# Kernel tuning notes

Hardware: AMD Instinct MI355X
Metric: run time of the kernel (lower is better)

Reference implementation:

```python
import jax, jax.numpy as jnp
import numpy as np

D_MODEL = 1024
N_HEADS = 16
D_K = D_MODEL // N_HEADS
MIN_F = 3
MAX_F = 10


def setup_inputs() -> dict:
    key = jax.random.key(0)
    ks = jax.random.split(key, 9)
    B, L = 4, 8192
    x = jax.random.normal(ks[0], (B, L, D_MODEL), jnp.float32)
    def w(k):
        return jax.random.normal(k, (D_MODEL, D_MODEL), jnp.float32) * 0.02
    def b(k):
        return jax.random.normal(k, (D_MODEL,), jnp.float32) * 0.02
    return {
        'x': x,
        'wq': w(ks[1]), 'bq': b(ks[2]),
        'wk': w(ks[3]), 'bk': b(ks[4]),
        'wv': w(ks[5]), 'bv': b(ks[6]),
        'wo': w(ks[7]), 'bo': b(ks[8]),
    }


def _sparsity_score(Q):
    # Q: (B, H, L, d_k)
    l2 = jnp.linalg.norm(Q, axis=-1)
    logp = jax.nn.log_softmax(Q, axis=-1)
    prob = jnp.exp(logp)
    entropy = -jnp.sum(prob * jnp.log(prob + 1e-9), axis=-1)
    var = jnp.var(Q, axis=-1, ddof=1)  # torch.var is unbiased by default
    return 0.5 * l2 + 0.3 * entropy + 0.2 * var


def reference(x, wq, bq, wk, bk, wv, bv, wo, bo):
    B, L, D = x.shape
    H, dk = N_HEADS, D_K
    # torch Linear: y = x @ W.T + b
    Q = (x @ wq.T + bq).reshape(B, L, H, dk).transpose(0, 2, 1, 3)  # (B,H,L,dk)
    K = (x @ wk.T + bk).reshape(B, L, H, dk).transpose(0, 2, 1, 3)
    V = (x @ wv.T + bv).reshape(B, L, H, dk).transpose(0, 2, 1, 3)

    q_scores = _sparsity_score(Q)  # (B,H,L)
    q_std = jnp.std(q_scores, axis=2, keepdims=True, ddof=1)
    q_mean = jnp.mean(q_scores, axis=2, keepdims=True)
    factor = jnp.clip(
        jnp.round(q_std / (q_mean + 1e-6) * MAX_F).astype(jnp.int32),
        MIN_F, MAX_F)  # (B,H,1)
    u = factor[:, 0, 0]  # per-batch k, taken from head 0 (matches torch code)

    # Fixed-size top-k of MAX_F; rows beyond u are masked to zero.
    _, top_idx = jax.lax.top_k(q_scores, MAX_F)  # (B,H,MAX_F)
    mask = (jnp.arange(MAX_F)[None, None, :] < u[:, None, None])  # (B,1->H,MAX_F)

    Q_sparse = jnp.take_along_axis(Q, top_idx[..., None], axis=2)  # (B,H,MAX_F,dk)
    scores = jnp.einsum('bhud,bhld->bhul', Q_sparse, K) / np.sqrt(dk).astype(np.float32)
    attn = jax.nn.softmax(scores, axis=-1)
    out = jnp.einsum('bhul,bhld->bhud', attn, V)  # (B,H,MAX_F,dk)
    out = out * mask[..., None].astype(out.dtype)

    # Scatter back into zeros; top-k indices are distinct per (b,h), so writing
    # masked zeros at the extra indices leaves those rows zero as in torch.
    bi = jnp.arange(B)[:, None, None]
    hi = jnp.arange(H)[None, :, None]
    full = jnp.zeros((B, H, L, dk), out.dtype).at[bi, hi, top_idx].set(out)

    merged = full.transpose(0, 2, 1, 3).reshape(B, L, D)
    return merged @ wo.T + bo
```

## Files before the change

### kernel.cpp

```cpp
#include <hip/hip_runtime.h>
#include <cmath>


typedef short     s16x8 __attribute__((ext_vector_type(8)));
typedef unsigned short u16x8 __attribute__((ext_vector_type(8)));
typedef unsigned short u16x4 __attribute__((ext_vector_type(4)));
typedef float     f32x4 __attribute__((ext_vector_type(4)));

__device__ __forceinline__ unsigned short f2bf(float f) {
    unsigned u = __float_as_uint(f);
    u += 0x7fffu + ((u >> 16) & 1u);
    return (unsigned short)(u >> 16);
}
__device__ __forceinline__ float bf2f(unsigned short s) {
    return __uint_as_float(((unsigned)s) << 16);
}

__device__ __forceinline__ void async16(const void* g, void* l) {
    __builtin_amdgcn_global_load_lds(
        (const __attribute__((address_space(1))) void*)g,
        (__attribute__((address_space(3))) void*)l, 16, 0, 0);
}

__global__ void k_conv(const float* __restrict__ x, const float* __restrict__ wq,
                       const float* __restrict__ wk, const float* __restrict__ wv,
                       unsigned short* __restrict__ xb, unsigned short* __restrict__ wb) {
    size_t i = (size_t)blockIdx.x * 256 + threadIdx.x;
    if (i < 8388608) {
        float4 v = ((const float4*)x)[i];
        ushort4 o; o.x = f2bf(v.x); o.y = f2bf(v.y); o.z = f2bf(v.z); o.w = f2bf(v.w);
        ((ushort4*)xb)[i] = o;
    } else {
        size_t j = i - 8388608;
        size_t wsel = j >> 18, rem = j & 262143;
        const float* src = wsel == 0 ? wq : (wsel == 1 ? wk : wv);
        float4 v = ((const float4*)src)[rem];
        ushort4 o; o.x = f2bf(v.x); o.y = f2bf(v.y); o.z = f2bf(v.z); o.w = f2bf(v.w);
        ((ushort4*)wb)[j] = o;
    }
}

__global__ __launch_bounds__(256) void k_gemm_qkv(
    const unsigned short* __restrict__ xb, const unsigned short* __restrict__ wb,
    const float* __restrict__ bq, const float* __restrict__ bk, const float* __restrict__ bv,
    unsigned short* __restrict__ Kb, unsigned short* __restrict__ Vb,
    float* __restrict__ scores)
{
    __shared__ unsigned short As[128 * 32];
    __shared__ unsigned short Bs[128 * 32];
    int bid = blockIdx.x;
    int mt = bid / 24, rem = bid % 24;
    int wsel = rem >> 3, nt = rem & 7;
    const unsigned short* wbase = wb + ((size_t)wsel << 20) + ((size_t)nt * 128) * 1024;
    const float* bias = wsel == 0 ? bq : (wsel == 1 ? bk : bv);
    unsigned short* outp = wsel == 1 ? Kb : Vb;
    int tid = threadIdx.x, wave = tid >> 6, lane = tid & 63;
    int ml = lane & 15, quad = lane >> 4, wm = wave >> 1, wn = wave & 1;
    int lr = lane >> 2, lc = lane & 3;
    const unsigned short* xbase = xb + ((size_t)mt * 128) * 1024;

    f32x4 acc[4][4] = {};
    for (int k0 = 0; k0 < 1024; k0 += 32) {
#pragma unroll
        for (int s = 0; s < 2; ++s) {
            int seg = wave * 2 + s;
            int row = seg * 16 + lr;
            async16(xbase + (size_t)row * 1024 + k0 + lc * 8, &As[seg * 512]);
            async16(wbase + (size_t)row * 1024 + k0 + lc * 8, &Bs[seg * 512]);
        }
        __builtin_amdgcn_s_waitcnt(0);
        __syncthreads();
        s16x8 a[4], b[4];
#pragma unroll
        for (int i = 0; i < 4; ++i) a[i] = *(const s16x8*)&As[(wm * 64 + i * 16 + ml) * 32 + quad * 8];
#pragma unroll
        for (int j = 0; j < 4; ++j) b[j] = *(const s16x8*)&Bs[(wn * 64 + j * 16 + ml) * 32 + quad * 8];
#pragma unroll
        for (int i = 0; i < 4; ++i)
#pragma unroll
            for (int j = 0; j < 4; ++j)
                acc[i][j] = __builtin_amdgcn_mfma_f32_16x16x32_bf16(a[i], b[j], acc[i][j], 0, 0, 0);
        __syncthreads();
    }

    float bvv[4];
#pragma unroll
    for (int j = 0; j < 4; ++j) bvv[j] = bias[nt * 128 + wn * 64 + j * 16 + ml];

    if (wsel == 0) {
        int hh = nt * 2 + wn;
#pragma unroll
        for (int i = 0; i < 4; ++i) {
#pragma unroll
            for (int r = 0; r < 4; ++r) {
                float q0 = acc[i][0][r] + bvv[0];
                float q1 = acc[i][1][r] + bvv[1];
                float q2 = acc[i][2][r] + bvv[2];
                float q3 = acc[i][3][r] + bvv[3];
                float mx = fmaxf(fmaxf(q0, q1), fmaxf(q2, q3));
                float sm = q0 + q1 + q2 + q3;
                float ss = q0 * q0 + q1 * q1 + q2 * q2 + q3 * q3;
#pragma unroll
                for (int off = 1; off < 16; off <<= 1) {
                    mx = fmaxf(mx, __shfl_xor(mx, off));
                    sm += __shfl_xor(sm, off);
                    ss += __shfl_xor(ss, off);
                }
                float e0 = expf(q0 - mx), e1 = expf(q1 - mx);
                float e2 = expf(q2 - mx), e3 = expf(q3 - mx);
                float S = e0 + e1 + e2 + e3;
#pragma unroll
                for (int off = 1; off < 16; off <<= 1) S += __shfl_xor(S, off);
                float is = 1.f / S;
                float p0 = e0 * is, p1 = e1 * is, p2 = e2 * is, p3 = e3 * is;
                float ent = -p0 * logf(p0 + 1e-9f) - p1 * logf(p1 + 1e-9f)
                            - p2 * logf(p2 + 1e-9f) - p3 * logf(p3 + 1e-9f);
                float mean = sm * (1.f / 64.f);
                float d0 = q0 - mean, d1 = q1 - mean, d2 = q2 - mean, d3 = q3 - mean;
                float var = d0 * d0 + d1 * d1 + d2 * d2 + d3 * d3;
#pragma unroll
                for (int off = 1; off < 16; off <<= 1) {
                    ent += __shfl_xor(ent, off);
                    var += __shfl_xor(var, off);
                }
                if (ml == 0) {
                    float sc = 0.5f * sqrtf(ss) + 0.3f * ent + 0.2f * (var * (1.f / 63.f));
                    int row = mt * 128 + wm * 64 + i * 16 + quad * 4 + r;
                    scores[(size_t)(((row >> 13) << 4) + hh) * 8192 + (row & 8191)] = sc;
                }
            }
        }
    } else {
#pragma unroll
        for (int i = 0; i < 4; ++i) {
            int grow0 = mt * 128 + wm * 64 + i * 16 + quad * 4;
#pragma unroll
            for (int j = 0; j < 4; ++j) {
                int gcol = nt * 128 + wn * 64 + j * 16 + ml;
#pragma unroll
                for (int r = 0; r < 4; ++r)
                    outp[(size_t)(grow0 + r) * 1024 + gcol] = f2bf(acc[i][j][r] + bvv[j]);
            }
        }
    }
}

__global__ __launch_bounds__(1024) void k_cand(const float* __restrict__ scores,
                                               int* __restrict__ cand, int* __restrict__ u)
{
    int pair = blockIdx.x; int t = threadIdx.x;
    __shared__ float  s_lds[8192];
    __shared__ double dred[1024];
    __shared__ float  wvv[16];
    __shared__ int    wii[16];
    const float* sp = scores + (size_t)pair * 8192;
    for (int i = t; i < 8192; i += 1024) s_lds[i] = sp[i];
    __syncthreads();

    if ((pair & 15) == 0) {
        double a0 = 0;
#pragma unroll
        for (int k = 0; k < 8; ++k) a0 += (double)s_lds[t + k * 1024];
        dred[t] = a0; __syncthreads();
        for (int st = 512; st > 0; st >>= 1) { if (t < st) dred[t] += dred[t + st]; __syncthreads(); }
        double mean = dred[0] / 8192.0;
        __syncthreads();
        double a1 = 0;
#pragma unroll
        for (int k = 0; k < 8; ++k) { double d = (double)s_lds[t + k * 1024] - mean; a1 += d * d; }
        dred[t] = a1; __syncthreads();
        for (int st = 512; st > 0; st >>= 1) { if (t < st) dred[t] += dred[t + st]; __syncthreads(); }
        if (t == 0) {
            double sd = sqrt(dred[0] / 8191.0);
            double ratio = sd / (mean + 1e-6) * 10.0;
            int f = (int)rint(ratio);
            f = f < 3 ? 3 : (f > 10 ? 10 : f);
            u[pair >> 4] = f;
        }
        __syncthreads();
    }

    for (int it = 0; it < 16; ++it) {
        float bv = -1e30f; int bi = 0x7fffffff;
#pragma unroll
        for (int k = 0; k < 8; ++k) {
            int i = t + k * 1024;
            float v = s_lds[i];
            if (v > bv || (v == bv && i < bi)) { bv = v; bi = i; }
        }
#pragma unroll
        for (int off = 32; off > 0; off >>= 1) {
            float ov = __shfl_down(bv, off);
            int   oi = __shfl_down(bi, off);
            if (ov > bv || (ov == bv && oi < bi)) { bv = ov; bi = oi; }
        }
        if ((t & 63) == 0) { wvv[t >> 6] = bv; wii[t >> 6] = bi; }
        __syncthreads();
        if (t == 0) {
            float fv = wvv[0]; int fi = wii[0];
            for (int k = 1; k < 16; ++k)
                if (wvv[k] > fv || (wvv[k] == fv && wii[k] < fi)) { fv = wvv[k]; fi = wii[k]; }
            cand[pair * 16 + it] = fi;
            s_lds[fi] = -1e30f;
        }
        __syncthreads();
    }
}

__global__ __launch_bounds__(256) void k_rescore(
    const int* __restrict__ cand, const float* __restrict__ x,
    const float* __restrict__ wq, const float* __restrict__ bq,
    double* __restrict__ cscore, float* __restrict__ cq)
{
    int bid = blockIdx.x;
    int pair = bid >> 4;
    int b = pair >> 4, h = pair & 15;
    int t = threadIdx.x;
    __shared__ float  xrow[1024];
    __shared__ double dred[256];
    __shared__ double qrow[64];

    int l = cand[bid];
    const float* xr = x + ((size_t)b * 8192 + l) * 1024;
    for (int i = t; i < 1024; i += 256) xrow[i] = xr[i];
    __syncthreads();

    int d = t >> 2, ks = t & 3;
    const float* wr = wq + (size_t)(h * 64 + d) * 1024 + ks * 256;
    const float* xs = xrow + ks * 256;
    double p = 0;
    for (int k = 0; k < 256; k += 4) {
        float4 w4 = *(const float4*)(wr + k);
        float4 x4 = *(const float4*)(xs + k);
        p += (double)w4.x * x4.x + (double)w4.y * x4.y +
             (double)w4.z * x4.z + (double)w4.w * x4.w;
    }
    dred[t] = p; __syncthreads();
    if ((t & 3) == 0)
        qrow[t >> 2] = dred[t] + dred[t + 1] + dred[t + 2] + dred[t + 3] + (double)bq[h * 64 + (t >> 2)];
    __syncthreads();

    if (t < 64) {
        double q = qrow[t];
        cq[(size_t)bid * 64 + t] = (float)q;
        double m = q;
#pragma unroll
        for (int off = 32; off > 0; off >>= 1) m = fmax(m, __shfl_down(m, off));
        m = __shfl(m, 0);
        double e = exp(q - m);
        double sum = q, sumsq = q * q, S = e;
#pragma unroll
        for (int off = 32; off > 0; off >>= 1) {
            sum += __shfl_down(sum, off);
            sumsq += __shfl_down(sumsq, off);
            S += __shfl_down(S, off);
        }
        sum = __shfl(sum, 0); sumsq = __shfl(sumsq, 0); S = __shfl(S, 0);
        double pp = e / S;
        double entc = -pp * log(pp + 1e-9);
        double mean = sum / 64.0;
        double dv = q - mean;
        double varc = dv * dv;
#pragma unroll
        for (int off = 32; off > 0; off >>= 1) {
            entc += __shfl_down(entc, off);
            varc += __shfl_down(varc, off);
        }
        if (t == 0)
            cscore[bid] = 0.5 * sqrt(sumsq) + 0.3 * entc + 0.2 * (varc / 63.0);
    }
}

__global__ void k_select(const int* __restrict__ cand, const double* __restrict__ cscore,
                         const float* __restrict__ cq,
                         int* __restrict__ sel, float* __restrict__ selq)
{
    int pair = blockIdx.x; int t = threadIdx.x;
    __shared__ int order[10];
    if (t == 0) {
        bool used[16] = {};
        for (int r = 0; r < 10; ++r) {
            int best = -1;
            for (int c = 0; c < 16; ++c) {
                if (used[c]) continue;
                int ic = pair * 16 + c;
                if (best < 0 || cscore[ic] > cscore[pair * 16 + best] ||
                    (cscore[ic] == cscore[pair * 16 + best] && cand[ic] < cand[pair * 16 + best]))
                    best = c;
            }
            used[best] = true; order[r] = best;
            sel[pair * 10 + r] = cand[pair * 16 + best];
        }
    }
    __syncthreads();
    for (int r = 0; r < 10; ++r)
        selq[((size_t)pair * 10 + r) * 64 + t] = cq[((size_t)pair * 16 + order[r]) * 64 + t];
}

__global__ __launch_bounds__(256) void k_attn_part(
    const unsigned short* __restrict__ Kb, const unsigned short* __restrict__ Vb,
    const float* __restrict__ selq, const int* __restrict__ u,
    float* __restrict__ part)
{
    int bid = blockIdx.x;
    int pair = bid >> 5, chunk = bid & 31;
    int b = pair >> 4, h = pair & 15;
    int uu = u[b];
    int t = threadIdx.x, wave = t >> 6, lane = t & 63;

    __shared__ float q_sh[10][64];
    __shared__ float w_sh[10][256];
    __shared__ unsigned short V_sh[256][68];
    __shared__ float mc_sh[10][2], Sc_sh[10][2];

    size_t kvbase = ((size_t)b * 8192 + (size_t)chunk * 256) * 1024 + h * 64;

    for (int i = t; i < uu * 64; i += 256)
        q_sh[i >> 6][i & 63] = selq[(size_t)pair * 640 + i] * 0.125f;

    const u16x8* kr = (const u16x8*)(Kb + kvbase + (size_t)t * 1024);
    const u16x8* vr = (const u16x8*)(Vb + kvbase + (size_t)t * 1024);
    u16x8 vreg[8];
#pragma unroll
    for (int k8 = 0; k8 < 8; ++k8) vreg[k8] = vr[k8];
#pragma unroll
    for (int k8 = 0; k8 < 8; ++k8) {
        *(u16x4*)&V_sh[t][k8 * 8]     = { vreg[k8][0], vreg[k8][1], vreg[k8][2], vreg[k8][3] };
        *(u16x4*)&V_sh[t][k8 * 8 + 4] = { vreg[k8][4], vreg[k8][5], vreg[k8][6], vreg[k8][7] };
    }
    float krow[64];
#pragma unroll
    for (int k8 = 0; k8 < 8; ++k8) {
        u16x8 kv = kr[k8];
#pragma unroll
        for (int e = 0; e < 8; ++e) krow[k8 * 8 + e] = bf2f(kv[e]);
    }
    __syncthreads();

    for (int rr = 0; rr < uu; ++rr) {
        const float4* qp = (const float4*)q_sh[rr];
        float acc = 0.f;
#pragma unroll
        for (int i4 = 0; i4 < 16; ++i4) {
            float4 q4 = qp[i4];
            acc += q4.x * krow[i4 * 4] + q4.y * krow[i4 * 4 + 1] +
                   q4.z * krow[i4 * 4 + 2] + q4.w * krow[i4 * 4 + 3];
        }
        w_sh[rr][t] = acc;
    }
    __syncthreads();

    for (int rr = wave; rr < uu; rr += 4) {
        float4 wv = *(const float4*)&w_sh[rr][lane * 4];
        float m4 = fmaxf(fmaxf(wv.x, wv.y), fmaxf(wv.z, wv.w));
#pragma unroll
        for (int off = 16; off > 0; off >>= 1) m4 = fmaxf(m4, __shfl_xor(m4, off));
        float e0 = expf(wv.x - m4), e1 = expf(wv.y - m4);
        float e2 = expf(wv.z - m4), e3 = expf(wv.w - m4);
        float s = e0 + e1 + e2 + e3;
#pragma unroll
        for (int off = 16; off > 0; off >>= 1) s += __shfl_xor(s, off);
        float4 ev = { e0, e1, e2, e3 };
        *(float4*)&w_sh[rr][lane * 4] = ev;
        if ((lane & 31) == 0) { int jh = lane >> 5; mc_sh[rr][jh] = m4; Sc_sh[rr][jh] = s; }
    }
    __syncthreads();

    int jh = t >> 7, tt = t & 127, dp = tt & 31;
    for (int rr = tt >> 5; rr < uu; rr += 4) {
        float o0 = 0.f, o1 = 0.f;
        int j0 = jh * 128;
        for (int j = j0; j < j0 + 128; j += 4) {
            float4 w4 = *(const float4*)&w_sh[rr][j];
#pragma unroll
            for (int jj = 0; jj < 4; ++jj) {
                unsigned v = *(const unsigned*)&V_sh[j + jj][dp * 2];
                float w1 = jj == 0 ? w4.x : (jj == 1 ? w4.y : (jj == 2 ? w4.z : w4.w));
                o0 += w1 * __uint_as_float(v << 16);
                o1 += w1 * __uint_as_float(v & 0xffff0000u);
            }
        }
        float* pp = part + (((size_t)pair * 10 + rr) * 64 + chunk * 2 + jh) * 66;
        float2 o2 = { o0, o1 };
        *(float2*)&pp[2 + dp * 2] = o2;
        if (dp == 0) { pp[0] = mc_sh[rr][jh]; pp[1] = Sc_sh[rr][jh]; }
    }
}

__global__ void k_bias(const float* __restrict__ bo, float* __restrict__ out) {
    size_t i = (size_t)blockIdx.x * 256 + threadIdx.x;
    int col4 = (int)(i & 255);
    ((float4*)out)[i] = ((const float4*)bo)[col4];
}

__global__ __launch_bounds__(256) void k_mergescatter(
    const float* __restrict__ part, const int* __restrict__ sel,
    const int* __restrict__ u, const float* __restrict__ wo,
    float* __restrict__ out)
{
    int idx = blockIdx.x; int pair = idx / 10; int r = idx % 10;
    int b = pair >> 4, h = pair & 15;
    if (r >= u[b]) return;
    int t = threadIdx.x;
    __shared__ float a_sh[64];
    if (t < 64) {
        const float* base = part + ((size_t)pair * 10 + r) * 64 * 66;
        float m = -1e30f;
        for (int c = 0; c < 64; ++c) m = fmaxf(m, base[c * 66]);
        float S = 0, o = 0;
        for (int c = 0; c < 64; ++c) {
            float f = expf(base[c * 66] - m);
            S += f * base[c * 66 + 1];
            o += f * base[c * 66 + 2 + t];
        }
        a_sh[t] = o / S;
    }
    __syncthreads();
    int l = sel[pair * 10 + r];
    float* orow = out + ((size_t)b * 8192 + l) * 1024;
    for (int j = t; j < 1024; j += 256) {
        const float* wr = wo + (size_t)j * 1024 + h * 64;
        float acc = 0;
#pragma unroll
        for (int d = 0; d < 64; d += 4) {
            float4 w4 = *(const float4*)(wr + d);
            acc += a_sh[d] * w4.x + a_sh[d + 1] * w4.y + a_sh[d + 2] * w4.z + a_sh[d + 3] * w4.w;
        }
        atomicAdd(orow + j, acc);
    }
}

static constexpr size_t OFF_XB    = 0;
static constexpr size_t OFF_WB    = OFF_XB + 67108864;
static constexpr size_t OFF_KB    = OFF_WB + 6291456;
static constexpr size_t OFF_VB    = OFF_KB + 67108864;
static constexpr size_t OFF_SC    = OFF_VB + 67108864;
static constexpr size_t OFF_U     = OFF_SC + 2097152;
static constexpr size_t OFF_SEL   = OFF_U + 256;
static constexpr size_t OFF_SELQ  = OFF_SEL + 4096;
static constexpr size_t OFF_PART  = OFF_SELQ + 163840;
static constexpr size_t OFF_CAND  = OFF_PART + 10813440;
static constexpr size_t OFF_CSC   = OFF_CAND + 4096;
static constexpr size_t OFF_CQ    = OFF_CSC + 8192;
static constexpr size_t WS_NEED   = OFF_CQ + 262144;

extern "C" void kernel_launch(void* const* d_in, const int* in_sizes, int n_in,
                              void* d_out, int out_size, void* d_ws, size_t ws_size,
                              hipStream_t stream)
{
    const float* x  = (const float*)d_in[0];
    const float* wq = (const float*)d_in[1];
    const float* bq = (const float*)d_in[2];
    const float* wk = (const float*)d_in[3];
    const float* bk = (const float*)d_in[4];
    const float* wv = (const float*)d_in[5];
    const float* bv = (const float*)d_in[6];
    const float* wo = (const float*)d_in[7];
    const float* bo = (const float*)d_in[8];
    float* out = (float*)d_out;

    if (ws_size < WS_NEED) return;

    char* ws = (char*)d_ws;
    unsigned short* xb = (unsigned short*)(ws + OFF_XB);
    unsigned short* wb = (unsigned short*)(ws + OFF_WB);
    unsigned short* Kb = (unsigned short*)(ws + OFF_KB);
    unsigned short* Vb = (unsigned short*)(ws + OFF_VB);
    float*  scores = (float*)(ws + OFF_SC);
    int*    u      = (int*)(ws + OFF_U);
    int*    sel    = (int*)(ws + OFF_SEL);
    float*  selq   = (float*)(ws + OFF_SELQ);
    float*  part   = (float*)(ws + OFF_PART);
    int*    cand   = (int*)(ws + OFF_CAND);
    double* cscore = (double*)(ws + OFF_CSC);
    float*  cq     = (float*)(ws + OFF_CQ);

    k_conv        <<<35840, 256,  0, stream>>>(x, wq, wk, wv, xb, wb);
    k_gemm_qkv    <<<6144,  256,  0, stream>>>(xb, wb, bq, bk, bv, Kb, Vb, scores);
    k_cand        <<<64,    1024, 0, stream>>>(scores, cand, u);
    k_rescore     <<<1024,  256,  0, stream>>>(cand, x, wq, bq, cscore, cq);
    k_select      <<<64,    64,   0, stream>>>(cand, cscore, cq, sel, selq);
    k_attn_part   <<<2048,  256,  0, stream>>>(Kb, Vb, selq, u, part);
    k_bias        <<<32768, 256,  0, stream>>>(bo, out);
    k_mergescatter<<<640,   256,  0, stream>>>(part, sel, u, wo, out);
}
```

Before: 728.4 us.

## Rewrite QKV GEMM with 256x256 tiles, swizzled double-buffered LDS pipeline

The QKV projection GEMM moves from 128x128 tiles with a single-buffered 32-wide K loop to 256x256 tiles with 512 threads, 64-wide K steps and 128 KB of dynamic LDS. The LDS is double-buffered, XOR-swizzled, and prefetches the next A and B slices in the middle of the MFMA phases, using s_setprio to favour the math. This is meant to raise arithmetic intensity, hide global-load latency and avoid LDS bank conflicts in the dominant GEMM. The cost is a large LDS footprint, which limits occupancy, plus more register pressure from 32 accumulators per wave.

```diff
diff --git a/kernel.cpp b/kernel.cpp
--- a/kernel.cpp
+++ b/kernel.cpp
@@ -40,74 +40,125 @@
     }
 }
 
-__global__ __launch_bounds__(256) void k_gemm_qkv(
+__global__ __launch_bounds__(512, 2) void k_gemm_qkv(
     const unsigned short* __restrict__ xb, const unsigned short* __restrict__ wb,
     const float* __restrict__ bq, const float* __restrict__ bk, const float* __restrict__ bv,
     unsigned short* __restrict__ Kb, unsigned short* __restrict__ Vb,
     float* __restrict__ scores)
 {
-    __shared__ unsigned short As[128 * 32];
-    __shared__ unsigned short Bs[128 * 32];
+    extern __shared__ char ldsb[];
     int bid = blockIdx.x;
-    int mt = bid / 24, rem = bid % 24;
-    int wsel = rem >> 3, nt = rem & 7;
-    const unsigned short* wbase = wb + ((size_t)wsel << 20) + ((size_t)nt * 128) * 1024;
+    int mt = bid / 12, ntile = bid % 12;
+    int wsel = ntile >> 2, ntq = ntile & 3;
+    int tid = threadIdx.x, wid = tid >> 6, lane = tid & 63;
+    int wm = wid >> 2, wn = wid & 3;
+    int ml = lane & 15, quad = lane >> 4;
+
+    const char* xg = (const char*)(xb + (size_t)mt * 256 * 1024);
+    const char* wg = (const char*)(wb + (size_t)ntile * 256 * 1024);
+
+    int rg0  = wid * 2;
+    int rsub = lane >> 3;
+    int cswz = ((lane & 7) ^ rsub) << 4;
+
+#define STAGE(gbase_, roff_) do {                                          \
+        const char* _g = (gbase_) + (size_t)(rg0 * 8 + rsub) * 2048 + cswz; \
+        char* _l = ldsb + (roff_) + rg0 * 1024;                             \
+        async16(_g, _l);                                                    \
+        async16(_g + 8 * 2048, _l + 1024);                                  \
+    } while (0)
+
+    int q0  = (quad * 16) ^ ((ml & 7) << 4);
+    int qk0 = q0, qk1 = q0 ^ 64;
+    int aconst = wm * 16384 + ml * 128;
+    int bconst = 32768 + (wn >> 1) * 16384 + (wn & 1) * 8192 + ml * 128;
+
+    f32x4 acc[8][4] = {};
+
+    STAGE(wg,                32768);
+    STAGE(wg + 262144,       32768 + 16384);
+    STAGE(xg,                0);
+    STAGE(xg + 262144,       16384);
+    STAGE(wg + 128,          65536 + 32768);
+    STAGE(wg + 262144 + 128, 65536 + 32768 + 16384);
+    asm volatile("s_waitcnt vmcnt(4)" ::: "memory");
+    __builtin_amdgcn_s_barrier();
+    asm volatile("" ::: "memory");
+
+    for (int t = 0; t < 16; ++t) {
+        int buf  = (t & 1) << 16;
+        int nbuf = buf ^ 65536;
+        const char* A_ = ldsb + buf + aconst;
+        const char* B_ = ldsb + buf + bconst;
+        s16x8 bfr[4][2];
+#pragma unroll
+        for (int p = 0; p < 4; ++p) {
+            if (p == 0) {
+#pragma unroll
+                for (int n = 0; n < 4; ++n) {
+                    bfr[n][0] = *(const s16x8*)(B_ + n * 2048 + qk0);
+                    bfr[n][1] = *(const s16x8*)(B_ + n * 2048 + qk1);
+                }
+            }
+            s16x8 am0[2], am1[2];
+            am0[0] = *(const s16x8*)(A_ + (2 * p) * 2048 + qk0);
+            am0[1] = *(const s16x8*)(A_ + (2 * p) * 2048 + qk1);
+            am1[0] = *(const s16x8*)(A_ + (2 * p + 1) * 2048 + qk0);
+            am1[1] = *(const s16x8*)(A_ + (2 * p + 1) * 2048 + qk1);
+            if (p == 0 && t < 15) STAGE(xg + (size_t)(t + 1) * 128, nbuf);
+            if (p == 1 && t < 15) STAGE(xg + 262144 + (size_t)(t + 1) * 128, nbuf + 16384);
+            if (p == 2 && t < 14) STAGE(wg + (size_t)(t + 2) * 128, buf + 32768);
+            if (p == 3 && t < 14) STAGE(wg + 262144 + (size_t)(t + 2) * 128, buf + 32768 + 16384);
+            asm volatile("" ::: "memory");
+            __builtin_amdgcn_s_barrier();
+            asm volatile("" ::: "memory");
+            __builtin_amdgcn_s_setprio(1);
+#pragma unroll
+            for (int kk = 0; kk < 2; ++kk)
+#pragma unroll
+                for (int n = 0; n < 4; ++n) {
+                    acc[2 * p][n]     = __builtin_amdgcn_mfma_f32_16x16x32_bf16(am0[kk], bfr[n][kk], acc[2 * p][n], 0, 0, 0);
+                    acc[2 * p + 1][n] = __builtin_amdgcn_mfma_f32_16x16x32_bf16(am1[kk], bfr[n][kk], acc[2 * p + 1][n], 0, 0, 0);
+                }
+            __builtin_amdgcn_s_setprio(0);
+            if (p == 3) {
+                if (t <= 13)      asm volatile("s_waitcnt vmcnt(4)" ::: "memory");
+                else if (t == 14) asm volatile("s_waitcnt vmcnt(0)" ::: "memory");
+            }
+            asm volatile("" ::: "memory");
+            __builtin_amdgcn_s_barrier();
+            asm volatile("" ::: "memory");
+        }
+    }
+#undef STAGE
+
+    float bvv[4];
     const float* bias = wsel == 0 ? bq : (wsel == 1 ? bk : bv);
-    unsigned short* outp = wsel == 1 ? Kb : Vb;
-    int tid = threadIdx.x, wave = tid >> 6, lane = tid & 63;
-    int ml = lane & 15, quad = lane >> 4, wm = wave >> 1, wn = wave & 1;
-    int lr = lane >> 2, lc = lane & 3;
-    const unsigned short* xbase = xb + ((size_t)mt * 128) * 1024;
-
-    f32x4 acc[4][4] = {};
-    for (int k0 = 0; k0 < 1024; k0 += 32) {
-#pragma unroll
-        for (int s = 0; s < 2; ++s) {
-            int seg = wave * 2 + s;
-            int row = seg * 16 + lr;
-            async16(xbase + (size_t)row * 1024 + k0 + lc * 8, &As[seg * 512]);
-            async16(wbase + (size_t)row * 1024 + k0 + lc * 8, &Bs[seg * 512]);
-        }
-        __builtin_amdgcn_s_waitcnt(0);
-        __syncthreads();
-        s16x8 a[4], b[4];
-#pragma unroll
-        for (int i = 0; i < 4; ++i) a[i] = *(const s16x8*)&As[(wm * 64 + i * 16 + ml) * 32 + quad * 8];
-#pragma unroll
-        for (int j = 0; j < 4; ++j) b[j] = *(const s16x8*)&Bs[(wn * 64 + j * 16 + ml) * 32 + quad * 8];
-#pragma unroll
-        for (int i = 0; i < 4; ++i)
-#pragma unroll
-            for (int j = 0; j < 4; ++j)
-                acc[i][j] = __builtin_amdgcn_mfma_f32_16x16x32_bf16(a[i], b[j], acc[i][j], 0, 0, 0);
-        __syncthreads();
-    }
-
-    float bvv[4];
-#pragma unroll
-    for (int j = 0; j < 4; ++j) bvv[j] = bias[nt * 128 + wn * 64 + j * 16 + ml];
+    int colbase = ntq * 256 + wn * 64;
+#pragma unroll
+    for (int n = 0; n < 4; ++n) bvv[n] = bias[colbase + n * 16 + ml];
 
     if (wsel == 0) {
-        int hh = nt * 2 + wn;
-#pragma unroll
-        for (int i = 0; i < 4; ++i) {
+        int hh = ntq * 4 + wn;
+#pragma unroll
+        for (int m = 0; m < 8; ++m) {
 #pragma unroll
             for (int r = 0; r < 4; ++r) {
-                float q0 = acc[i][0][r] + bvv[0];
-                float q1 = acc[i][1][r] + bvv[1];
-                float q2 = acc[i][2][r] + bvv[2];
-                float q3 = acc[i][3][r] + bvv[3];
-                float mx = fmaxf(fmaxf(q0, q1), fmaxf(q2, q3));
-                float sm = q0 + q1 + q2 + q3;
-                float ss = q0 * q0 + q1 * q1 + q2 * q2 + q3 * q3;
+                float q0v = acc[m][0][r] + bvv[0];
+                float q1v = acc[m][1][r] + bvv[1];
+                float q2v = acc[m][2][r] + bvv[2];
+                float q3v = acc[m][3][r] + bvv[3];
+                float mx = fmaxf(fmaxf(q0v, q1v), fmaxf(q2v, q3v));
+                float sm = q0v + q1v + q2v + q3v;
+                float ss = q0v * q0v + q1v * q1v + q2v * q2v + q3v * q3v;
 #pragma unroll
                 for (int off = 1; off < 16; off <<= 1) {
                     mx = fmaxf(mx, __shfl_xor(mx, off));
                     sm += __shfl_xor(sm, off);
                     ss += __shfl_xor(ss, off);
                 }
-                float e0 = expf(q0 - mx), e1 = expf(q1 - mx);
-                float e2 = expf(q2 - mx), e3 = expf(q3 - mx);
+                float e0 = expf(q0v - mx), e1 = expf(q1v - mx);
+                float e2 = expf(q2v - mx), e3 = expf(q3v - mx);
                 float S = e0 + e1 + e2 + e3;
 #pragma unroll
                 for (int off = 1; off < 16; off <<= 1) S += __shfl_xor(S, off);
@@ -116,7 +167,7 @@
                 float ent = -p0 * logf(p0 + 1e-9f) - p1 * logf(p1 + 1e-9f)
                             - p2 * logf(p2 + 1e-9f) - p3 * logf(p3 + 1e-9f);
                 float mean = sm * (1.f / 64.f);
-                float d0 = q0 - mean, d1 = q1 - mean, d2 = q2 - mean, d3 = q3 - mean;
+                float d0 = q0v - mean, d1 = q1v - mean, d2 = q2v - mean, d3 = q3v - mean;
                 float var = d0 * d0 + d1 * d1 + d2 * d2 + d3 * d3;
 #pragma unroll
                 for (int off = 1; off < 16; off <<= 1) {
@@ -125,21 +176,22 @@
                 }
                 if (ml == 0) {
                     float sc = 0.5f * sqrtf(ss) + 0.3f * ent + 0.2f * (var * (1.f / 63.f));
-                    int row = mt * 128 + wm * 64 + i * 16 + quad * 4 + r;
+                    int row = mt * 256 + wm * 128 + m * 16 + quad * 4 + r;
                     scores[(size_t)(((row >> 13) << 4) + hh) * 8192 + (row & 8191)] = sc;
                 }
             }
         }
     } else {
-#pragma unroll
-        for (int i = 0; i < 4; ++i) {
-            int grow0 = mt * 128 + wm * 64 + i * 16 + quad * 4;
-#pragma unroll
-            for (int j = 0; j < 4; ++j) {
-                int gcol = nt * 128 + wn * 64 + j * 16 + ml;
+        unsigned short* outp = wsel == 1 ? Kb : Vb;
+#pragma unroll
+        for (int m = 0; m < 8; ++m) {
+            int grow0 = mt * 256 + wm * 128 + m * 16 + quad * 4;
+#pragma unroll
+            for (int n = 0; n < 4; ++n) {
+                int gcol = colbase + n * 16 + ml;
 #pragma unroll
                 for (int r = 0; r < 4; ++r)
-                    outp[(size_t)(grow0 + r) * 1024 + gcol] = f2bf(acc[i][j][r] + bvv[j]);
+                    outp[(size_t)(grow0 + r) * 1024 + gcol] = f2bf(acc[m][n][r] + bvv[n]);
             }
         }
     }
@@ -475,12 +527,12 @@
     double* cscore = (double*)(ws + OFF_CSC);
     float*  cq     = (float*)(ws + OFF_CQ);
 
-    k_conv        <<<35840, 256,  0, stream>>>(x, wq, wk, wv, xb, wb);
-    k_gemm_qkv    <<<6144,  256,  0, stream>>>(xb, wb, bq, bk, bv, Kb, Vb, scores);
-    k_cand        <<<64,    1024, 0, stream>>>(scores, cand, u);
-    k_rescore     <<<1024,  256,  0, stream>>>(cand, x, wq, bq, cscore, cq);
-    k_select      <<<64,    64,   0, stream>>>(cand, cscore, cq, sel, selq);
-    k_attn_part   <<<2048,  256,  0, stream>>>(Kb, Vb, selq, u, part);
-    k_bias        <<<32768, 256,  0, stream>>>(bo, out);
-    k_mergescatter<<<640,   256,  0, stream>>>(part, sel, u, wo, out);
-}
+    k_conv        <<<35840, 256,  0,      stream>>>(x, wq, wk, wv, xb, wb);
+    k_gemm_qkv    <<<1536,  512,  131072, stream>>>(xb, wb, bq, bk, bv, Kb, Vb, scores);
+    k_cand        <<<64,    1024, 0,      stream>>>(scores, cand, u);
+    k_rescore     <<<1024,  256,  0,      stream>>>(cand, x, wq, bq, cscore, cq);
+    k_select      <<<64,    64,   0,      stream>>>(cand, cscore, cq, sel, selq);
+    k_attn_part   <<<2048,  256,  0,      stream>>>(Kb, Vb, selq, u, part);
+    k_bias        <<<32768, 256,  0,      stream>>>(bo, out);
+    k_mergescatter<<<640,   256,  0,      stream>>>(part, sel, u, wo, out);
+}
```

New measurement: 759.9 us. 4.3% more time.

## Widen QKV GEMM K-tile to 64 with swizzled LDS, parallelize candidate selection

Applied to the files above, without the earlier changes.

The QKV projection GEMM now loads a 64-wide K slice per iteration into a single 32KB LDS buffer. The layout uses an XOR swizzle on 16-byte column chunks to avoid bank conflicts, halving the number of barrier round-trips per tile, and occupancy is hinted at 3 blocks per CU. The top-10 candidate selection replaces a serial single-thread loop with a 16-lane shuffle argmax reduction. The larger LDS footprint may limit occupancy, and the tie-breaking in the shuffle reduction must match the original ordering.

```diff
diff --git a/kernel.cpp b/kernel.cpp
--- a/kernel.cpp
+++ b/kernel.cpp
@@ -40,47 +40,65 @@
     }
 }
 
-__global__ __launch_bounds__(256) void k_gemm_qkv(
+__global__ __launch_bounds__(256, 3) void k_gemm_qkv(
     const unsigned short* __restrict__ xb, const unsigned short* __restrict__ wb,
     const float* __restrict__ bq, const float* __restrict__ bk, const float* __restrict__ bv,
     unsigned short* __restrict__ Kb, unsigned short* __restrict__ Vb,
     float* __restrict__ scores)
 {
-    __shared__ unsigned short As[128 * 32];
-    __shared__ unsigned short Bs[128 * 32];
+    __shared__ __align__(16) char lds[32768];
     int bid = blockIdx.x;
     int mt = bid / 24, rem = bid % 24;
     int wsel = rem >> 3, nt = rem & 7;
-    const unsigned short* wbase = wb + ((size_t)wsel << 20) + ((size_t)nt * 128) * 1024;
+    const char* wg = (const char*)(wb + ((size_t)wsel << 20) + (size_t)nt * 128 * 1024);
+    const char* xg = (const char*)(xb + (size_t)mt * 128 * 1024);
     const float* bias = wsel == 0 ? bq : (wsel == 1 ? bk : bv);
-    unsigned short* outp = wsel == 1 ? Kb : Vb;
-    int tid = threadIdx.x, wave = tid >> 6, lane = tid & 63;
-    int ml = lane & 15, quad = lane >> 4, wm = wave >> 1, wn = wave & 1;
-    int lr = lane >> 2, lc = lane & 3;
-    const unsigned short* xbase = xb + ((size_t)mt * 128) * 1024;
+    int tid = threadIdx.x, wid = tid >> 6, lane = tid & 63;
+    int wm = wid >> 1, wn = wid & 1;
+    int ml = lane & 15, quad = lane >> 4;
+
+    int srow = tid >> 3;
+    int scol = ((tid & 7) ^ (srow & 7)) << 4;
+
+    int qk0  = (quad ^ (ml & 7)) << 4;
+    int aoff = (wm * 64 + ml) * 128;
+    int boff = 16384 + (wn * 64 + ml) * 128;
 
     f32x4 acc[4][4] = {};
-    for (int k0 = 0; k0 < 1024; k0 += 32) {
-#pragma unroll
-        for (int s = 0; s < 2; ++s) {
-            int seg = wave * 2 + s;
-            int row = seg * 16 + lr;
-            async16(xbase + (size_t)row * 1024 + k0 + lc * 8, &As[seg * 512]);
-            async16(wbase + (size_t)row * 1024 + k0 + lc * 8, &Bs[seg * 512]);
-        }
-        __builtin_amdgcn_s_waitcnt(0);
-        __syncthreads();
-        s16x8 a[4], b[4];
-#pragma unroll
-        for (int i = 0; i < 4; ++i) a[i] = *(const s16x8*)&As[(wm * 64 + i * 16 + ml) * 32 + quad * 8];
-#pragma unroll
-        for (int j = 0; j < 4; ++j) b[j] = *(const s16x8*)&Bs[(wn * 64 + j * 16 + ml) * 32 + quad * 8];
-#pragma unroll
-        for (int i = 0; i < 4; ++i)
-#pragma unroll
-            for (int j = 0; j < 4; ++j)
-                acc[i][j] = __builtin_amdgcn_mfma_f32_16x16x32_bf16(a[i], b[j], acc[i][j], 0, 0, 0);
-        __syncthreads();
+
+    for (int kt = 0; kt < 16; ++kt) {
+#pragma unroll
+        for (int p = 0; p < 4; ++p)
+            async16(xg + (size_t)(p * 32 + srow) * 2048 + kt * 128 + scol,
+                    lds + p * 4096 + tid * 16);
+#pragma unroll
+        for (int p = 0; p < 4; ++p)
+            async16(wg + (size_t)(p * 32 + srow) * 2048 + kt * 128 + scol,
+                    lds + 16384 + p * 4096 + tid * 16);
+        asm volatile("s_waitcnt vmcnt(0)" ::: "memory");
+        __builtin_amdgcn_s_barrier();
+        asm volatile("" ::: "memory");
+        s16x8 a[4][2], b[4][2];
+#pragma unroll
+        for (int i = 0; i < 4; ++i) {
+            a[i][0] = *(const s16x8*)&lds[aoff + i * 2048 + qk0];
+            a[i][1] = *(const s16x8*)&lds[aoff + i * 2048 + (qk0 ^ 64)];
+        }
+#pragma unroll
+        for (int j = 0; j < 4; ++j) {
+            b[j][0] = *(const s16x8*)&lds[boff + j * 2048 + qk0];
+            b[j][1] = *(const s16x8*)&lds[boff + j * 2048 + (qk0 ^ 64)];
+        }
+#pragma unroll
+        for (int kk = 0; kk < 2; ++kk)
+#pragma unroll
+            for (int i = 0; i < 4; ++i)
+#pragma unroll
+                for (int j = 0; j < 4; ++j)
+                    acc[i][j] = __builtin_amdgcn_mfma_f32_16x16x32_bf16(a[i][kk], b[j][kk], acc[i][j], 0, 0, 0);
+        asm volatile("" ::: "memory");
+        __builtin_amdgcn_s_barrier();
+        asm volatile("" ::: "memory");
     }
 
     float bvv[4];
@@ -131,6 +149,7 @@
             }
         }
     } else {
+        unsigned short* outp = wsel == 1 ? Kb : Vb;
 #pragma unroll
         for (int i = 0; i < 4; ++i) {
             int grow0 = mt * 128 + wm * 64 + i * 16 + quad * 4;
@@ -277,20 +296,19 @@
 {
     int pair = blockIdx.x; int t = threadIdx.x;
     __shared__ int order[10];
-    if (t == 0) {
-        bool used[16] = {};
-        for (int r = 0; r < 10; ++r) {
-            int best = -1;
-            for (int c = 0; c < 16; ++c) {
-                if (used[c]) continue;
-                int ic = pair * 16 + c;
-                if (best < 0 || cscore[ic] > cscore[pair * 16 + best] ||
-                    (cscore[ic] == cscore[pair * 16 + best] && cand[ic] < cand[pair * 16 + best]))
-                    best = c;
-            }
-            used[best] = true; order[r] = best;
-            sel[pair * 10 + r] = cand[pair * 16 + best];
-        }
+    double sc = t < 16 ? cscore[pair * 16 + t] : -1.0e300;
+    int    ci = t < 16 ? cand[pair * 16 + t]   : 0x7fffffff;
+    for (int r = 0; r < 10; ++r) {
+        double bs = sc; int bi = ci; int bc = t & 15;
+#pragma unroll
+        for (int off = 8; off > 0; off >>= 1) {
+            double os = __shfl_xor(bs, off);
+            int    oi = __shfl_xor(bi, off);
+            int    oc = __shfl_xor(bc, off);
+            if (os > bs || (os == bs && oi < bi)) { bs = os; bi = oi; bc = oc; }
+        }
+        if (t == 0) { order[r] = bc; sel[pair * 10 + r] = bi; }
+        if ((t & 15) == bc && t < 16) { sc = -1.0e300; ci = 0x7fffffff; }
     }
     __syncthreads();
     for (int r = 0; r < 10; ++r)
```

Measured after the change: 701.8 us. 3.7% less time.
